# Optimization experiments

Measured on AMD Instinct MI355X. Metric: run time of the kernel, lower is better.

The kernel has to match this reference:

```python
import jax, jax.numpy as jnp
import numpy as np
from jax import lax

T, B, D = 2048, 16, 1024


def setup_inputs() -> dict:
    key = jax.random.key(0)
    ks = jax.random.split(key, 3)
    xavier = (6.0 / (D + D)) ** 0.5  # xavier_uniform bound
    x = jax.random.normal(ks[0], (T, B, D), dtype=jnp.float32)
    W_alpha = jax.random.uniform(ks[1], (D, D), jnp.float32, -xavier, xavier)
    W_x = jax.random.uniform(ks[2], (D, D), jnp.float32, -xavier, xavier)
    b_alpha = jnp.full((D,), 2.0, jnp.float32)  # init_alpha_bias
    d_g = jnp.full((D,), 0.5, jnp.float32)      # init_d_g
    b_g = jnp.full((D,), 0.5, jnp.float32)      # init_b_g
    b_v = jnp.zeros((D,), jnp.float32)
    return {"x": x, "W_alpha": W_alpha, "b_alpha": b_alpha, "d_g": d_g,
            "b_g": b_g, "W_x": W_x, "b_v": b_v}


def reference(x, W_alpha, b_alpha, d_g, b_g, W_x, b_v):
    Tn, Bn, Dn = x.shape
    # Batched input projections (as in the torch code, done before the loop)
    alpha_all = jax.nn.sigmoid(jnp.einsum('tbd,ed->tbe', x, W_alpha) + b_alpha)  # [T,B,D]
    v_raw_all = jnp.tanh(jnp.einsum('tbd,ed->tbe', x, W_x) + b_v)                # [T,B,D]

    h0 = jnp.zeros((Bn, Dn), x.dtype)

    def step(h_prev, inp):
        alpha, v_raw = inp
        g = jax.nn.sigmoid(-d_g * jnp.abs(h_prev) + b_g)  # inverse self-gating
        v = v_raw * g
        h_new = alpha * h_prev + (1.0 - alpha) * v
        out = h_new * jax.nn.silu(h_new)
        return h_new, (h_new, out)

    _, (hs, outs) = lax.scan(step, h0, (alpha_all, v_raw_all))
    h = jnp.concatenate([h0[None], hs], axis=0)  # [T+1,B,D]
    return outs, h
```

## Files before the change

kernel.cpp:

```cpp
#include <hip/hip_runtime.h>
#include <hip/hip_fp16.h>

#define T_DIM 2048
#define B_DIM 16
#define D_DIM 1024
#define M_TOT (T_DIM * B_DIM)
#define N_TOT (2 * D_DIM)
#define K_TOT D_DIM
#define BD    (B_DIM * D_DIM)

typedef __attribute__((ext_vector_type(8))) short short8;
typedef __attribute__((ext_vector_type(4))) float floatx4;

__device__ __forceinline__ short f32_to_bf16(float f) {
  unsigned u = __float_as_uint(f);
  u = (u + 0x7FFFu + ((u >> 16) & 1u)) >> 16;
  return (short)u;
}

__global__ __launch_bounds__(256) void cast_bf16_k(const float* __restrict__ src,
                                                   short* __restrict__ dst) {
  const size_t i = ((size_t)blockIdx.x * 256 + threadIdx.x) * 8;
  floatx4 f0 = *(const floatx4*)(src + i);
  floatx4 f1 = *(const floatx4*)(src + i + 4);
  short8 o;
  o[0] = f32_to_bf16(f0[0]); o[1] = f32_to_bf16(f0[1]);
  o[2] = f32_to_bf16(f0[2]); o[3] = f32_to_bf16(f0[3]);
  o[4] = f32_to_bf16(f1[0]); o[5] = f32_to_bf16(f1[1]);
  o[6] = f32_to_bf16(f1[2]); o[7] = f32_to_bf16(f1[3]);
  *(short8*)(dst + i) = o;
}

#define GLDS16(gp, lp)                                                                   \
  __builtin_amdgcn_global_load_lds((const __attribute__((address_space(1))) void*)(gp),  \
                                   (__attribute__((address_space(3))) void*)(lp), 16, 0, 0)

__global__ __launch_bounds__(256, 2) void gemm_act_k(
    const short* __restrict__ xb, const short* __restrict__ wb,
    const float* __restrict__ b_alpha, const float* __restrict__ b_v,
    __half* __restrict__ pairbuf) {
  __shared__ __align__(16) short As[128 * 32];
  __shared__ __align__(16) short Bs[128 * 32];
  const int tid  = threadIdx.x;
  const int wave = tid >> 6;
  const int lane = tid & 63;
  const int quad = lane >> 4;
  const int l16  = lane & 15;
  const int mblk = blockIdx.y << 7;
  const int nblk = blockIdx.x << 7;
  const int wrow = (wave >> 1) << 6;
  const int wcol = (wave & 1) << 6;

  floatx4 acc[4][4];
#pragma unroll
  for (int i = 0; i < 4; ++i)
#pragma unroll
    for (int j = 0; j < 4; ++j) acc[i][j] = {0.f, 0.f, 0.f, 0.f};

  const int chunk_m = tid >> 2;
  const int c_swz   = (tid & 3) ^ (chunk_m & 3) ^ ((chunk_m >> 2) & 1);
  const short* gA0 = xb + (size_t)(mblk + chunk_m) * K_TOT + c_swz * 8;
  const short* gA1 = gA0 + (size_t)64 * K_TOT;
  const short* gB0 = wb + (size_t)(nblk + chunk_m) * K_TOT + c_swz * 8;
  const short* gB1 = gB0 + (size_t)64 * K_TOT;
  short* lA0 = As + wave * 512;
  short* lA1 = As + 2048 + wave * 512;
  short* lB0 = Bs + wave * 512;
  short* lB1 = Bs + 2048 + wave * 512;

  const int pl   = (l16 & 3) ^ ((l16 >> 2) & 1);
  const int aoff = (wrow + l16) * 32 + ((quad ^ pl) * 8);
  const int boff = (wcol + l16) * 32 + ((quad ^ pl) * 8);

  for (int k0 = 0; k0 < K_TOT; k0 += 32) {
    GLDS16(gA0 + k0, lA0);
    GLDS16(gA1 + k0, lA1);
    GLDS16(gB0 + k0, lB0);
    GLDS16(gB1 + k0, lB1);
    __syncthreads();
    short8 af[4], bf[4];
#pragma unroll
    for (int i = 0; i < 4; ++i) af[i] = *(const short8*)(As + aoff + i * 512);
#pragma unroll
    for (int i = 0; i < 4; ++i) bf[i] = *(const short8*)(Bs + boff + i * 512);
#pragma unroll
    for (int i = 0; i < 4; ++i)
#pragma unroll
      for (int j = 0; j < 4; ++j)
        acc[i][j] = __builtin_amdgcn_mfma_f32_16x16x32_bf16(af[i], bf[j], acc[i][j], 0, 0, 0);
    __syncthreads();
  }

  const bool isA = (nblk < D_DIM);
  const float* __restrict__ bias = isA ? b_alpha : b_v;
  const int hsel = isA ? 0 : 1;
#pragma unroll
  for (int j = 0; j < 4; ++j) {
    const int n_g = nblk + wcol + j * 16 + l16;
    const int e = isA ? n_g : (n_g - D_DIM);
    const float bz = bias[e];
#pragma unroll
    for (int i = 0; i < 4; ++i) {
      const floatx4 v = acc[i][j];
      const int m_base = mblk + wrow + i * 16 + quad * 4;
#pragma unroll
      for (int r = 0; r < 4; ++r) {
        const float z = v[r] + bz;
        float val;
        if (isA) {
          val = __builtin_amdgcn_rcpf(1.f + __expf(-z));
        } else {
          val = 1.f - 2.f * __builtin_amdgcn_rcpf(__expf(2.f * z) + 1.f);
        }
        pairbuf[((size_t)(m_base + r) * D_DIM + e) * 2 + hsel] = __float2half(val);
      }
    }
  }
}

__global__ __launch_bounds__(64) void scan_k(const __half2* __restrict__ pair,
                                             const float* __restrict__ d_g,
                                             const float* __restrict__ b_g,
                                             __half* __restrict__ hh) {
  const int c = blockIdx.x * 64 + threadIdx.x;
  const float LOG2E = 1.44269504f;
  const float dg = d_g[c & (D_DIM - 1)] * LOG2E;
  const float bg = b_g[c & (D_DIM - 1)] * LOG2E;
  hh[c] = __float2half(0.f);
  float h = 0.f;
  size_t idx = c;
  __half2 p[16];
#pragma unroll
  for (int k = 0; k < 16; ++k) p[k] = pair[idx + (size_t)k * BD];
  for (int t = 0; t < T_DIM; t += 16) {
    const size_t pfadd = (t + 16 < T_DIM) ? (size_t)16 * BD : 0;
#pragma unroll
    for (int k = 0; k < 16; ++k) {
      const float2 av = __half22float2(p[k]);
      p[k] = pair[idx + pfadd];
      const float w = (1.f - av.x) * av.y;
      const float e = __builtin_amdgcn_exp2f(fmaf(dg, fabsf(h), -bg));
      const float g = __builtin_amdgcn_rcpf(1.f + e);
      h = fmaf(av.x, h, w * g);
      hh[idx + BD] = __float2half(h);
      idx += BD;
    }
  }
}

__global__ __launch_bounds__(256) void silu_k(const __half* __restrict__ hh,
                                              float* __restrict__ outbuf) {
  const float LOG2E = 1.44269504f;
  const size_t i = ((size_t)blockIdx.x * 256 + threadIdx.x) * 8;
  float* __restrict__ outs = outbuf;
  float* __restrict__ hout = outbuf + (size_t)T_DIM * BD;
  const __half2* hp = (const __half2*)(hh + i);
  float hf[8];
#pragma unroll
  for (int j = 0; j < 4; ++j) {
    const float2 f = __half22float2(hp[j]);
    hf[2 * j] = f.x; hf[2 * j + 1] = f.y;
  }
  *(floatx4*)(hout + i)     = floatx4{hf[0], hf[1], hf[2], hf[3]};
  *(floatx4*)(hout + i + 4) = floatx4{hf[4], hf[5], hf[6], hf[7]};
  if (i >= BD) {
    float o[8];
#pragma unroll
    for (int j = 0; j < 8; ++j) {
      const float s = __builtin_amdgcn_rcpf(1.f + __builtin_amdgcn_exp2f(-LOG2E * hf[j]));
      o[j] = hf[j] * hf[j] * s;
    }
    *(floatx4*)(outs + i - BD)     = floatx4{o[0], o[1], o[2], o[3]};
    *(floatx4*)(outs + i - BD + 4) = floatx4{o[4], o[5], o[6], o[7]};
  }
}

extern "C" void kernel_launch(void* const* d_in, const int* in_sizes, int n_in,
                              void* d_out, int out_size, void* d_ws, size_t ws_size,
                              hipStream_t stream) {
  const float* x       = (const float*)d_in[0];
  const float* W_alpha = (const float*)d_in[1];
  const float* b_alpha = (const float*)d_in[2];
  const float* d_g     = (const float*)d_in[3];
  const float* b_g     = (const float*)d_in[4];
  const float* W_x     = (const float*)d_in[5];
  const float* b_v     = (const float*)d_in[6];
  float* out = (float*)d_out;

  char* ws = (char*)d_ws;
  short*  xb      = (short*)ws;
  short*  wb      = (short*)(ws + (size_t)67108864);
  __half* pairbuf = (__half*)(ws + (size_t)71303168);
  __half* h_half  = (__half*)ws;

  cast_bf16_k<<<M_TOT * K_TOT / (8 * 256), 256, 0, stream>>>(x, xb);
  cast_bf16_k<<<D_DIM * K_TOT / (8 * 256), 256, 0, stream>>>(W_alpha, wb);
  cast_bf16_k<<<D_DIM * K_TOT / (8 * 256), 256, 0, stream>>>(W_x, wb + (size_t)D_DIM * K_TOT);
  gemm_act_k<<<dim3(N_TOT / 128, M_TOT / 128), 256, 0, stream>>>(xb, wb, b_alpha, b_v, pairbuf);
  scan_k<<<BD / 64, 64, 0, stream>>>((const __half2*)pairbuf, d_g, b_g, h_half);
  silu_k<<<(T_DIM + 1) * BD / (8 * 256), 256, 0, stream>>>(h_half, out);
}
```

Before: 673.8 us.

## Interleave alpha/v GEMM columns, load B from global, merge casts, deepen scan prefetch

The three cast launches become one kernel over a concatenated index space. The GEMM now gives each block 64 features of both W_alpha and W_x, so alpha and tanh(v) are computed together and written as one half2 store instead of scattered half stores. B fragments are read directly from global memory into registers, with no LDS staging, and the LDS swizzle on A is dropped. The scan prefetch depth goes from 16 to 32 steps. Together these aim to cut launch overhead and the strided epilogue writes. The risks are LDS bank conflicts on A, uncoalesced or poorly cached global B loads, and higher register pressure in the scan.

```diff
diff --git a/kernel.cpp b/kernel.cpp
--- a/kernel.cpp
+++ b/kernel.cpp
@@ -5,9 +5,10 @@
 #define B_DIM 16
 #define D_DIM 1024
 #define M_TOT (T_DIM * B_DIM)
-#define N_TOT (2 * D_DIM)
 #define K_TOT D_DIM
 #define BD    (B_DIM * D_DIM)
+#define XN    ((size_t)M_TOT * K_TOT)
+#define WN    ((size_t)D_DIM * K_TOT)
 
 typedef __attribute__((ext_vector_type(8))) short short8;
 typedef __attribute__((ext_vector_type(4))) float floatx4;
@@ -18,17 +19,23 @@
   return (short)u;
 }
 
-__global__ __launch_bounds__(256) void cast_bf16_k(const float* __restrict__ src,
-                                                   short* __restrict__ dst) {
+__global__ __launch_bounds__(256) void cast_all_k(const float* __restrict__ x,
+                                                  const float* __restrict__ Wa,
+                                                  const float* __restrict__ Wx,
+                                                  short* __restrict__ xb) {
   const size_t i = ((size_t)blockIdx.x * 256 + threadIdx.x) * 8;
-  floatx4 f0 = *(const floatx4*)(src + i);
-  floatx4 f1 = *(const floatx4*)(src + i + 4);
+  const float* src; size_t si;
+  if (i < XN)           { src = x;  si = i; }
+  else if (i < XN + WN) { src = Wa; si = i - XN; }
+  else                  { src = Wx; si = i - XN - WN; }
+  floatx4 f0 = *(const floatx4*)(src + si);
+  floatx4 f1 = *(const floatx4*)(src + si + 4);
   short8 o;
   o[0] = f32_to_bf16(f0[0]); o[1] = f32_to_bf16(f0[1]);
   o[2] = f32_to_bf16(f0[2]); o[3] = f32_to_bf16(f0[3]);
   o[4] = f32_to_bf16(f1[0]); o[5] = f32_to_bf16(f1[1]);
   o[6] = f32_to_bf16(f1[2]); o[7] = f32_to_bf16(f1[3]);
-  *(short8*)(dst + i) = o;
+  *(short8*)(xb + i) = o;
 }
 
 #define GLDS16(gp, lp)                                                                   \
@@ -38,16 +45,15 @@
 __global__ __launch_bounds__(256, 2) void gemm_act_k(
     const short* __restrict__ xb, const short* __restrict__ wb,
     const float* __restrict__ b_alpha, const float* __restrict__ b_v,
-    __half* __restrict__ pairbuf) {
+    __half2* __restrict__ pairbuf) {
   __shared__ __align__(16) short As[128 * 32];
-  __shared__ __align__(16) short Bs[128 * 32];
   const int tid  = threadIdx.x;
   const int wave = tid >> 6;
   const int lane = tid & 63;
   const int quad = lane >> 4;
   const int l16  = lane & 15;
   const int mblk = blockIdx.y << 7;
-  const int nblk = blockIdx.x << 7;
+  const int eblk = blockIdx.x << 6;
   const int wrow = (wave >> 1) << 6;
   const int wcol = (wave & 1) << 6;
 
@@ -58,31 +64,30 @@
     for (int j = 0; j < 4; ++j) acc[i][j] = {0.f, 0.f, 0.f, 0.f};
 
   const int chunk_m = tid >> 2;
-  const int c_swz   = (tid & 3) ^ (chunk_m & 3) ^ ((chunk_m >> 2) & 1);
-  const short* gA0 = xb + (size_t)(mblk + chunk_m) * K_TOT + c_swz * 8;
+  const short* gA0 = xb + (size_t)(mblk + chunk_m) * K_TOT + (tid & 3) * 8;
   const short* gA1 = gA0 + (size_t)64 * K_TOT;
-  const short* gB0 = wb + (size_t)(nblk + chunk_m) * K_TOT + c_swz * 8;
-  const short* gB1 = gB0 + (size_t)64 * K_TOT;
   short* lA0 = As + wave * 512;
   short* lA1 = As + 2048 + wave * 512;
-  short* lB0 = Bs + wave * 512;
-  short* lB1 = Bs + 2048 + wave * 512;
-
-  const int pl   = (l16 & 3) ^ ((l16 >> 2) & 1);
-  const int aoff = (wrow + l16) * 32 + ((quad ^ pl) * 8);
-  const int boff = (wcol + l16) * 32 + ((quad ^ pl) * 8);
+  const int aoff = (wrow + l16) * 32 + quad * 8;
+
+  const short* gB[4];
+#pragma unroll
+  for (int j = 0; j < 4; ++j) {
+    const int g = (wcol >> 4) + j;
+    const int row = (g & 1) * D_DIM + eblk + ((g >> 1) << 4) + l16;
+    gB[j] = wb + (size_t)row * K_TOT + quad * 8;
+  }
 
   for (int k0 = 0; k0 < K_TOT; k0 += 32) {
+    short8 bf[4];
+#pragma unroll
+    for (int j = 0; j < 4; ++j) bf[j] = *(const short8*)(gB[j] + k0);
     GLDS16(gA0 + k0, lA0);
     GLDS16(gA1 + k0, lA1);
-    GLDS16(gB0 + k0, lB0);
-    GLDS16(gB1 + k0, lB1);
     __syncthreads();
-    short8 af[4], bf[4];
+    short8 af[4];
 #pragma unroll
     for (int i = 0; i < 4; ++i) af[i] = *(const short8*)(As + aoff + i * 512);
-#pragma unroll
-    for (int i = 0; i < 4; ++i) bf[i] = *(const short8*)(Bs + boff + i * 512);
 #pragma unroll
     for (int i = 0; i < 4; ++i)
 #pragma unroll
@@ -91,28 +96,24 @@
     __syncthreads();
   }
 
-  const bool isA = (nblk < D_DIM);
-  const float* __restrict__ bias = isA ? b_alpha : b_v;
-  const int hsel = isA ? 0 : 1;
-#pragma unroll
-  for (int j = 0; j < 4; ++j) {
-    const int n_g = nblk + wcol + j * 16 + l16;
-    const int e = isA ? n_g : (n_g - D_DIM);
-    const float bz = bias[e];
+#pragma unroll
+  for (int p = 0; p < 2; ++p) {
+    const int e = eblk + (wcol >> 1) + p * 16 + l16;
+    const float ba = b_alpha[e];
+    const float bv = b_v[e];
 #pragma unroll
     for (int i = 0; i < 4; ++i) {
-      const floatx4 v = acc[i][j];
+      const floatx4 va = acc[i][2 * p];
+      const floatx4 vv = acc[i][2 * p + 1];
       const int m_base = mblk + wrow + i * 16 + quad * 4;
 #pragma unroll
       for (int r = 0; r < 4; ++r) {
-        const float z = v[r] + bz;
-        float val;
-        if (isA) {
-          val = __builtin_amdgcn_rcpf(1.f + __expf(-z));
-        } else {
-          val = 1.f - 2.f * __builtin_amdgcn_rcpf(__expf(2.f * z) + 1.f);
-        }
-        pairbuf[((size_t)(m_base + r) * D_DIM + e) * 2 + hsel] = __float2half(val);
+        const float za = va[r] + ba;
+        const float zv = vv[r] + bv;
+        const float alpha = __builtin_amdgcn_rcpf(1.f + __expf(-za));
+        const float vtanh = 1.f - 2.f * __builtin_amdgcn_rcpf(__expf(2.f * zv) + 1.f);
+        pairbuf[(size_t)(m_base + r) * D_DIM + e] =
+            __halves2half2(__float2half(alpha), __float2half(vtanh));
       }
     }
   }
@@ -129,13 +130,13 @@
   hh[c] = __float2half(0.f);
   float h = 0.f;
   size_t idx = c;
-  __half2 p[16];
-#pragma unroll
-  for (int k = 0; k < 16; ++k) p[k] = pair[idx + (size_t)k * BD];
-  for (int t = 0; t < T_DIM; t += 16) {
-    const size_t pfadd = (t + 16 < T_DIM) ? (size_t)16 * BD : 0;
-#pragma unroll
-    for (int k = 0; k < 16; ++k) {
+  __half2 p[32];
+#pragma unroll
+  for (int k = 0; k < 32; ++k) p[k] = pair[idx + (size_t)k * BD];
+  for (int t = 0; t < T_DIM; t += 32) {
+    const size_t pfadd = (t + 32 < T_DIM) ? (size_t)32 * BD : 0;
+#pragma unroll
+    for (int k = 0; k < 32; ++k) {
       const float2 av = __half22float2(p[k]);
       p[k] = pair[idx + pfadd];
       const float w = (1.f - av.x) * av.y;
@@ -188,15 +189,13 @@
   float* out = (float*)d_out;
 
   char* ws = (char*)d_ws;
-  short*  xb      = (short*)ws;
-  short*  wb      = (short*)(ws + (size_t)67108864);
-  __half* pairbuf = (__half*)(ws + (size_t)71303168);
-  __half* h_half  = (__half*)ws;
-
-  cast_bf16_k<<<M_TOT * K_TOT / (8 * 256), 256, 0, stream>>>(x, xb);
-  cast_bf16_k<<<D_DIM * K_TOT / (8 * 256), 256, 0, stream>>>(W_alpha, wb);
-  cast_bf16_k<<<D_DIM * K_TOT / (8 * 256), 256, 0, stream>>>(W_x, wb + (size_t)D_DIM * K_TOT);
-  gemm_act_k<<<dim3(N_TOT / 128, M_TOT / 128), 256, 0, stream>>>(xb, wb, b_alpha, b_v, pairbuf);
-  scan_k<<<BD / 64, 64, 0, stream>>>((const __half2*)pairbuf, d_g, b_g, h_half);
+  short*   xb      = (short*)ws;
+  short*   wb      = (short*)(ws + (size_t)67108864);
+  __half2* pairbuf = (__half2*)(ws + (size_t)71303168);
+  __half*  h_half  = (__half*)ws;
+
+  cast_all_k<<<(XN + 2 * WN) / (8 * 256), 256, 0, stream>>>(x, W_alpha, W_x, xb);
+  gemm_act_k<<<dim3(D_DIM / 64, M_TOT / 128), 256, 0, stream>>>(xb, wb, b_alpha, b_v, pairbuf);
+  scan_k<<<BD / 64, 64, 0, stream>>>(pairbuf, d_g, b_g, h_half);
   silu_k<<<(T_DIM + 1) * BD / (8 * 256), 256, 0, stream>>>(h_half, out);
 }
```

New measurement: 766.2 us. 1.14x slower.
